# Performance work log

Measured on AMD Instinct MI355X. Metric: run time of the kernel, lower is better.

The kernel has to match this reference:

```python
import jax, jax.numpy as jnp
import numpy as np

N_EMBD = 448
HEAD_SIZE = 64

def setup_inputs() -> dict:
    key = jax.random.key(0)
    k1, k2, k3, k4 = jax.random.split(key, 4)
    B, T = 16, 2048
    x = jax.random.normal(k1, (B, T, N_EMBD), dtype=jnp.float32)
    # nn.Linear(n_embd, head_size, bias=False): weight shape (head_size, n_embd); y = x @ W.T
    s = 1.0 / np.sqrt(N_EMBD)
    Wk = jax.random.uniform(k2, (HEAD_SIZE, N_EMBD), jnp.float32, -s, s)
    Wq = jax.random.uniform(k3, (HEAD_SIZE, N_EMBD), jnp.float32, -s, s)
    Wv = jax.random.uniform(k4, (HEAD_SIZE, N_EMBD), jnp.float32, -s, s)
    return {"x": x, "Wk": Wk, "Wq": Wq, "Wv": Wv}

def reference(x, Wk, Wq, Wv):
    B, T, C = x.shape
    k = jnp.einsum('btc,hc->bth', x, Wk)  # (B,T,H)
    q = jnp.einsum('btc,hc->bth', x, Wq)
    v = jnp.einsum('btc,hc->bth', x, Wv)
    scale = 1.0 / jnp.sqrt(jnp.float32(C))  # NOTE: scales by sqrt(n_embd), as in source
    wei = jnp.einsum('bth,bsh->bts', q, k) * scale  # (B,T,T)
    causal = jnp.tril(jnp.ones((T, T), dtype=bool))
    wei = jnp.where(causal[None, :, :], wei, -jnp.inf)
    wei = jax.nn.softmax(wei, axis=-1)
    # dropout is identity in eval mode
    out = jnp.einsum('bts,bsh->bth', wei, v)  # (B,T,H)
    return out
```

## Files before the change

### kernel.cpp

```cpp
#include <hip/hip_runtime.h>
#include <math.h>

#define BT 32768
#define NC 448
#define NH 64
#define TT 2048

typedef __bf16 bf16x8 __attribute__((ext_vector_type(8)));
typedef float  f32x4  __attribute__((ext_vector_type(4)));

__device__ __forceinline__ unsigned short f2bf(float f) {
  unsigned u = __builtin_bit_cast(unsigned, f);
  return (unsigned short)((u + 0x7FFFu + ((u >> 16) & 1u)) >> 16);
}
__device__ __forceinline__ ushort4 f2bf4(float4 v) {
  ushort4 b; b.x = f2bf(v.x); b.y = f2bf(v.y); b.z = f2bf(v.z); b.w = f2bf(v.w);
  return b;
}
__device__ __forceinline__ float bf2f(unsigned short u) {
  return __builtin_bit_cast(float, (unsigned)u << 16);
}


__global__ __launch_bounds__(256) void proj_kernel(
    const float* __restrict__ x, const float* __restrict__ Wk,
    const float* __restrict__ Wq, const float* __restrict__ Wv,
    unsigned short* __restrict__ kws, unsigned short* __restrict__ qws,
    unsigned short* __restrict__ vws)
{
  __shared__ unsigned short xs[2][4096];
  __shared__ unsigned short wsm[2][4096];
  const int tid = threadIdx.x;
  const int w = tid >> 6, lane = tid & 63;
  const int q = lane >> 4, l15 = lane & 15;
  const int r0 = blockIdx.x * 64;
  const int p = blockIdx.y;
  const float* W = (p == 0) ? Wk : ((p == 1) ? Wq : Wv);

  f32x4 acc[4];
#pragma unroll
  for (int i = 0; i < 4; ++i) acc[i] = f32x4{0.f, 0.f, 0.f, 0.f};

  const int c0 = (tid & 15) * 4, r_ = tid >> 4;

  float4 xr[4], wr[4];
#pragma unroll
  for (int i = 0; i < 4; ++i) {
    xr[i] = *(const float4*)&x[(size_t)(r0 + r_ + 16 * i) * NC + c0];
    wr[i] = *(const float4*)&W[(size_t)(r_ + 16 * i) * NC + c0];
  }

  for (int ch = 0; ch < 7; ++ch) {
    const int cur = ch & 1;
#pragma unroll
    for (int i = 0; i < 4; ++i) {
      int r = r_ + 16 * i;
      int off = r * 64 + (((c0 >> 3) ^ (r & 7)) << 3) + (c0 & 7);
      *(ushort4*)&xs[cur][off]  = f2bf4(xr[i]);
      *(ushort4*)&wsm[cur][off] = f2bf4(wr[i]);
    }
    __syncthreads();
    if (ch < 6) {
      int kc = (ch + 1) * 64;
#pragma unroll
      for (int i = 0; i < 4; ++i) {
        xr[i] = *(const float4*)&x[(size_t)(r0 + r_ + 16 * i) * NC + kc + c0];
        wr[i] = *(const float4*)&W[(size_t)(r_ + 16 * i) * NC + kc + c0];
      }
    }
#pragma unroll
    for (int ks = 0; ks < 2; ++ks) {
      int xrow = w * 16 + l15;
      int g = q + 4 * ks;
      bf16x8 xf = *(const bf16x8*)&xs[cur][xrow * 64 + ((g ^ (xrow & 7)) << 3)];
#pragma unroll
      for (int t = 0; t < 4; ++t) {
        int wrow = t * 16 + l15;
        bf16x8 wf = *(const bf16x8*)&wsm[cur][wrow * 64 + ((g ^ (wrow & 7)) << 3)];
        if (p == 0)
          acc[t] = __builtin_amdgcn_mfma_f32_16x16x32_bf16(wf, xf, acc[t], 0, 0, 0);
        else
          acc[t] = __builtin_amdgcn_mfma_f32_16x16x32_bf16(xf, wf, acc[t], 0, 0, 0);
      }
    }
  }

  const size_t tile = (size_t)blockIdx.x * 4096;
  if (p == 0) {
#pragma unroll
    for (int t = 0; t < 4; ++t) {
      int j = w * 16 + l15;
      ushort4 bb; bb.x = f2bf(acc[t][0]); bb.y = f2bf(acc[t][1]);
      bb.z = f2bf(acc[t][2]); bb.w = f2bf(acc[t][3]);
      *(ushort4*)&kws[tile + j * 64 + (((2 * t + (q >> 1)) ^ (j & 7)) << 3) + ((q & 1) << 2)] = bb;
    }
  } else if (p == 1) {
    const float qs = 0.068161075f;
#pragma unroll
    for (int t = 0; t < 4; ++t) {
      int h = t * 16 + l15;
#pragma unroll
      for (int rr = 0; rr < 4; ++rr) {
        int R = r0 + w * 16 + q * 4 + rr;
        qws[(size_t)R * 64 + h] = f2bf(acc[t][rr] * qs);
      }
    }
  } else {
#pragma unroll
    for (int t = 0; t < 4; ++t) {
      int h = t * 16 + l15;
      ushort4 bb; bb.x = f2bf(acc[t][0]); bb.y = f2bf(acc[t][1]);
      bb.z = f2bf(acc[t][2]); bb.w = f2bf(acc[t][3]);
      *(ushort4*)&vws[tile + h * 64 + (((2 * w + (q >> 1)) ^ (h & 7)) << 3) + ((q & 1) << 2)] = bb;
    }
  }
}

__global__ __launch_bounds__(256) void attn_partial(
    const unsigned short* __restrict__ kws, const unsigned short* __restrict__ qws,
    const unsigned short* __restrict__ vws, float* __restrict__ out,
    unsigned short* __restrict__ opart, float* __restrict__ mlpart)
{
  __shared__ unsigned short ksm[2][4096];
  __shared__ unsigned short vtm[2][4096];
  __shared__ unsigned short psm[4096];
  const int bx = blockIdx.x, b = blockIdx.y;
  int qt, kt0, ktn, ci; bool direct;
  if (bx < 16)      { qt = 16 + bx; kt0 = 0;  ktn = 16;     ci = 0; direct = false; }
  else if (bx < 32) { qt = 47 - bx; kt0 = 16; ktn = qt + 1; ci = 1; direct = false; }
  else              { qt = 47 - bx; kt0 = 0;  ktn = qt + 1; ci = 0; direct = true;  }
  const int nt = ktn - kt0;

  const int tid = threadIdx.x;
  const int w = tid >> 6, lane = tid & 63;
  const int q = lane >> 4, l15 = lane & 15;
  const int t0 = b * TT + qt * 64;
  const int l7 = l15 & 7;

  bf16x8 qf[2];
#pragma unroll
  for (int ks = 0; ks < 2; ++ks)
    qf[ks] = *(const bf16x8*)&qws[(size_t)(t0 + w * 16 + l15) * 64 + 32 * ks + q * 8];

  f32x4 oacc[4];
#pragma unroll
  for (int ht = 0; ht < 4; ++ht) oacc[ht] = f32x4{0.f, 0.f, 0.f, 0.f};
  float m_i = -INFINITY, l_i = 0.f;

  uint4 kr0, kr1, vr0, vr1;
  {
    const unsigned short* kt_ = kws + (size_t)(b * 32 + kt0) * 4096;
    const unsigned short* vt_ = vws + (size_t)(b * 32 + kt0) * 4096;
    kr0 = *(const uint4*)&kt_[tid * 8];  kr1 = *(const uint4*)&kt_[2048 + tid * 8];
    vr0 = *(const uint4*)&vt_[tid * 8];  vr1 = *(const uint4*)&vt_[2048 + tid * 8];
  }

  for (int it = 0; it < nt; ++it) {
    const int kt = kt0 + it;
    const int cur = it & 1;
    *(uint4*)&ksm[cur][tid * 8] = kr0;  *(uint4*)&ksm[cur][2048 + tid * 8] = kr1;
    *(uint4*)&vtm[cur][tid * 8] = vr0;  *(uint4*)&vtm[cur][2048 + tid * 8] = vr1;
    __syncthreads();
    if (it + 1 < nt) {
      const unsigned short* kt_ = kws + (size_t)(b * 32 + kt + 1) * 4096;
      const unsigned short* vt_ = vws + (size_t)(b * 32 + kt + 1) * 4096;
      kr0 = *(const uint4*)&kt_[tid * 8];  kr1 = *(const uint4*)&kt_[2048 + tid * 8];
      vr0 = *(const uint4*)&vt_[tid * 8];  vr1 = *(const uint4*)&vt_[2048 + tid * 8];
    }

    f32x4 sacc[4];
#pragma unroll
    for (int jt = 0; jt < 4; ++jt) sacc[jt] = f32x4{0.f, 0.f, 0.f, 0.f};
#pragma unroll
    for (int jt = 0; jt < 4; ++jt) {
      int j = jt * 16 + l15;
#pragma unroll
      for (int ks = 0; ks < 2; ++ks) {
        bf16x8 kf = *(const bf16x8*)&ksm[cur][j * 64 + (((q + 4 * ks) ^ (j & 7)) << 3)];
        sacc[jt] = __builtin_amdgcn_mfma_f32_16x16x32_bf16(kf, qf[ks], sacc[jt], 0, 0, 0);
      }
    }

    if (kt == qt) {
      int iloc = w * 16 + l15;
#pragma unroll
      for (int jt = 0; jt < 4; ++jt)
#pragma unroll
        for (int rr = 0; rr < 4; ++rr)
          if (jt * 16 + q * 4 + rr > iloc) sacc[jt][rr] = -INFINITY;
    }

    float mx = -INFINITY;
#pragma unroll
    for (int jt = 0; jt < 4; ++jt)
#pragma unroll
      for (int rr = 0; rr < 4; ++rr) mx = fmaxf(mx, sacc[jt][rr]);
    mx = fmaxf(mx, __shfl_xor(mx, 16));
    mx = fmaxf(mx, __shfl_xor(mx, 32));
    float mn = fmaxf(m_i, mx);
    float alpha = exp2f(m_i - mn);
    m_i = mn;
    float p[4][4], rs = 0.f;
#pragma unroll
    for (int jt = 0; jt < 4; ++jt)
#pragma unroll
      for (int rr = 0; rr < 4; ++rr) {
        float pv = exp2f(sacc[jt][rr] - mn);
        p[jt][rr] = pv; rs += pv;
      }
    rs += __shfl_xor(rs, 16);
    rs += __shfl_xor(rs, 32);
    l_i = l_i * alpha + rs;

    float a_t[4];
#pragma unroll
    for (int rr = 0; rr < 4; ++rr) a_t[rr] = __shfl(alpha, q * 4 + rr);
#pragma unroll
    for (int ht = 0; ht < 4; ++ht)
#pragma unroll
      for (int rr = 0; rr < 4; ++rr) oacc[ht][rr] *= a_t[rr];

    {
      int row = w * 16 + l15;
#pragma unroll
      for (int jt = 0; jt < 4; ++jt) {
        ushort4 bb; bb.x = f2bf(p[jt][0]); bb.y = f2bf(p[jt][1]);
        bb.z = f2bf(p[jt][2]); bb.w = f2bf(p[jt][3]);
        *(ushort4*)&psm[row * 64 + (((2 * jt + (q >> 1)) ^ l7) << 3) + ((q & 1) << 2)] = bb;
      }
    }

#pragma unroll
    for (int ks2 = 0; ks2 < 2; ++ks2) {
      int prow = w * 16 + l15;
      bf16x8 pf = *(const bf16x8*)&psm[prow * 64 + (((q + 4 * ks2) ^ l7) << 3)];
#pragma unroll
      for (int ht = 0; ht < 4; ++ht) {
        int h = ht * 16 + l15;
        bf16x8 vf = *(const bf16x8*)&vtm[cur][h * 64 + (((q + 4 * ks2) ^ l7) << 3)];
        oacc[ht] = __builtin_amdgcn_mfma_f32_16x16x32_bf16(pf, vf, oacc[ht], 0, 0, 0);
      }
    }
  }

  if (direct) {
    float l_t[4];
#pragma unroll
    for (int rr = 0; rr < 4; ++rr) l_t[rr] = __shfl(l_i, q * 4 + rr);
#pragma unroll
    for (int rr = 0; rr < 4; ++rr) {
      float inv = 1.f / l_t[rr];
      int R = t0 + w * 16 + q * 4 + rr;
#pragma unroll
      for (int ht = 0; ht < 4; ++ht)
        out[(size_t)R * 64 + ht * 16 + l15] = oacc[ht][rr] * inv;
    }
  } else {
    const size_t slot = (size_t)(b * 16 + (qt - 16)) * 2 + ci;
    unsigned short* Op = opart + slot * 4096;
#pragma unroll
    for (int rr = 0; rr < 4; ++rr) {
      int rloc = w * 16 + q * 4 + rr;
#pragma unroll
      for (int ht = 0; ht < 4; ++ht)
        Op[rloc * 64 + ht * 16 + l15] = f2bf(oacc[ht][rr]);
    }
    if (q == 0) {
      mlpart[slot * 128 + w * 16 + l15]      = m_i;
      mlpart[slot * 128 + 64 + w * 16 + l15] = l_i;
    }
  }
}

__global__ __launch_bounds__(256) void combine_kernel(
    const unsigned short* __restrict__ opart, const float* __restrict__ mlpart,
    float* __restrict__ out)
{
  const int qtc = blockIdx.x, b = blockIdx.y;
  const int qt = 16 + qtc;
  const int t = threadIdx.x;
  const int r = t >> 2, c0 = (t & 3) * 16;
  const size_t s0 = (size_t)(b * 16 + qtc) * 2;

  float m0 = mlpart[s0 * 128 + r],       l0 = mlpart[s0 * 128 + 64 + r];
  float m1 = mlpart[(s0 + 1) * 128 + r], l1 = mlpart[(s0 + 1) * 128 + 64 + r];
  float m  = fmaxf(m0, m1);
  float w0 = exp2f(m0 - m), w1 = exp2f(m1 - m);
  float inv = 1.f / (w0 * l0 + w1 * l1);
  w0 *= inv; w1 *= inv;

  const unsigned short* O0 = opart + s0 * 4096 + r * 64 + c0;
  const unsigned short* O1 = opart + (s0 + 1) * 4096 + r * 64 + c0;
  union { uint4 v; unsigned short e[8]; } a0, a1;
  float* op = out + (size_t)(b * TT + qt * 64 + r) * 64;
#pragma unroll
  for (int half = 0; half < 2; ++half) {
    a0.v = *(const uint4*)&O0[half * 8];
    a1.v = *(const uint4*)&O1[half * 8];
    float res[8];
#pragma unroll
    for (int u = 0; u < 8; ++u)
      res[u] = w0 * bf2f(a0.e[u]) + w1 * bf2f(a1.e[u]);
    *(float4*)&op[c0 + half * 8]     = make_float4(res[0], res[1], res[2], res[3]);
    *(float4*)&op[c0 + half * 8 + 4] = make_float4(res[4], res[5], res[6], res[7]);
  }
}

extern "C" void kernel_launch(void* const* d_in, const int* in_sizes, int n_in,
                              void* d_out, int out_size, void* d_ws, size_t ws_size,
                              hipStream_t stream) {
  const float* x  = (const float*)d_in[0];
  const float* Wk = (const float*)d_in[1];
  const float* Wq = (const float*)d_in[2];
  const float* Wv = (const float*)d_in[3];
  unsigned short* kws = (unsigned short*)d_ws;
  unsigned short* qws = kws + (size_t)BT * NH;
  unsigned short* vws = qws + (size_t)BT * NH;
  unsigned short* opart = vws + (size_t)BT * NH;
  float* mlpart = (float*)(opart + (size_t)512 * 4096);
  float* out = (float*)d_out;

  proj_kernel<<<dim3(512, 3), 256, 0, stream>>>(x, Wk, Wq, Wv, kws, qws, vws);
  attn_partial<<<dim3(48, 16), 256, 0, stream>>>(kws, qws, vws, out, opart, mlpart);
  combine_kernel<<<dim3(16, 16), 256, 0, stream>>>(opart, mlpart, out);
}
```

Baseline: 147.7 us.

## Fuse K/Q/V projections into one pass over x with prepacked bf16 weights

The projection kernel previously ran three grid slices, each reading and converting the same x tile for one weight matrix. Now one block computes all three projections from a single x tile in shared memory. A new small kernel prepacks the weights into bf16 fragment order so each wave loads its weight fragments straight into registers, which removes the weight staging through shared memory. The cost is an extra kernel launch, roughly three times more accumulator registers, fewer blocks (512 instead of 1536), and reuse of the opart workspace as scratch for the packed weights.

```diff
diff --git a/kernel.cpp b/kernel.cpp
--- a/kernel.cpp
+++ b/kernel.cpp
@@ -22,33 +22,53 @@
 }
 
 
+__global__ __launch_bounds__(256) void wprep_kernel(
+    const float* __restrict__ Wk, const float* __restrict__ Wq,
+    const float* __restrict__ Wv, unsigned short* __restrict__ wp)
+{
+  int idx = blockIdx.x * 256 + threadIdx.x;
+  int r = idx & 63;
+  int t = idx >> 6;
+  int g = t & 7; t >>= 3;
+  int ch = t % 7, p = t / 7;
+  const float* W = (p == 0) ? Wk : ((p == 1) ? Wq : Wv);
+  const float* src = &W[(size_t)r * NC + ch * 64 + g * 8];
+  float4 a = *(const float4*)src;
+  float4 b = *(const float4*)(src + 4);
+  *(ushort4*)&wp[(size_t)idx * 8]     = f2bf4(a);
+  *(ushort4*)&wp[(size_t)idx * 8 + 4] = f2bf4(b);
+}
+
 __global__ __launch_bounds__(256) void proj_kernel(
-    const float* __restrict__ x, const float* __restrict__ Wk,
-    const float* __restrict__ Wq, const float* __restrict__ Wv,
+    const float* __restrict__ x, const unsigned short* __restrict__ wp,
     unsigned short* __restrict__ kws, unsigned short* __restrict__ qws,
     unsigned short* __restrict__ vws)
 {
   __shared__ unsigned short xs[2][4096];
-  __shared__ unsigned short wsm[2][4096];
   const int tid = threadIdx.x;
   const int w = tid >> 6, lane = tid & 63;
   const int q = lane >> 4, l15 = lane & 15;
   const int r0 = blockIdx.x * 64;
-  const int p = blockIdx.y;
-  const float* W = (p == 0) ? Wk : ((p == 1) ? Wq : Wv);
-
-  f32x4 acc[4];
-#pragma unroll
-  for (int i = 0; i < 4; ++i) acc[i] = f32x4{0.f, 0.f, 0.f, 0.f};
+
+  f32x4 acc[3][4];
+#pragma unroll
+  for (int p = 0; p < 3; ++p)
+#pragma unroll
+    for (int t = 0; t < 4; ++t) acc[p][t] = f32x4{0.f, 0.f, 0.f, 0.f};
 
   const int c0 = (tid & 15) * 4, r_ = tid >> 4;
-
-  float4 xr[4], wr[4];
-#pragma unroll
-  for (int i = 0; i < 4; ++i) {
+  const int wbase = (w * 16 + l15) * 8;
+
+  float4 xr[4];
+  bf16x8 wfr[3][2], wnx[3][2];
+#pragma unroll
+  for (int i = 0; i < 4; ++i)
     xr[i] = *(const float4*)&x[(size_t)(r0 + r_ + 16 * i) * NC + c0];
-    wr[i] = *(const float4*)&W[(size_t)(r_ + 16 * i) * NC + c0];
-  }
+#pragma unroll
+  for (int p = 0; p < 3; ++p)
+#pragma unroll
+    for (int ks = 0; ks < 2; ++ks)
+      wfr[p][ks] = *(const bf16x8*)&wp[(size_t)((p * 7 + 0) * 8 + (q + 4 * ks)) * 512 + wbase];
 
   for (int ch = 0; ch < 7; ++ch) {
     const int cur = ch & 1;
@@ -56,62 +76,66 @@
     for (int i = 0; i < 4; ++i) {
       int r = r_ + 16 * i;
       int off = r * 64 + (((c0 >> 3) ^ (r & 7)) << 3) + (c0 & 7);
-      *(ushort4*)&xs[cur][off]  = f2bf4(xr[i]);
-      *(ushort4*)&wsm[cur][off] = f2bf4(wr[i]);
+      *(ushort4*)&xs[cur][off] = f2bf4(xr[i]);
     }
     __syncthreads();
     if (ch < 6) {
       int kc = (ch + 1) * 64;
 #pragma unroll
-      for (int i = 0; i < 4; ++i) {
+      for (int i = 0; i < 4; ++i)
         xr[i] = *(const float4*)&x[(size_t)(r0 + r_ + 16 * i) * NC + kc + c0];
-        wr[i] = *(const float4*)&W[(size_t)(r_ + 16 * i) * NC + kc + c0];
-      }
+#pragma unroll
+      for (int p = 0; p < 3; ++p)
+#pragma unroll
+        for (int ks = 0; ks < 2; ++ks)
+          wnx[p][ks] = *(const bf16x8*)&wp[(size_t)((p * 7 + ch + 1) * 8 + (q + 4 * ks)) * 512 + wbase];
     }
 #pragma unroll
     for (int ks = 0; ks < 2; ++ks) {
-      int xrow = w * 16 + l15;
-      int g = q + 4 * ks;
-      bf16x8 xf = *(const bf16x8*)&xs[cur][xrow * 64 + ((g ^ (xrow & 7)) << 3)];
 #pragma unroll
       for (int t = 0; t < 4; ++t) {
-        int wrow = t * 16 + l15;
-        bf16x8 wf = *(const bf16x8*)&wsm[cur][wrow * 64 + ((g ^ (wrow & 7)) << 3)];
-        if (p == 0)
-          acc[t] = __builtin_amdgcn_mfma_f32_16x16x32_bf16(wf, xf, acc[t], 0, 0, 0);
-        else
-          acc[t] = __builtin_amdgcn_mfma_f32_16x16x32_bf16(xf, wf, acc[t], 0, 0, 0);
-      }
+        int xrow = t * 16 + l15;
+        bf16x8 xf = *(const bf16x8*)&xs[cur][xrow * 64 + (((q + 4 * ks) ^ (xrow & 7)) << 3)];
+        acc[0][t] = __builtin_amdgcn_mfma_f32_16x16x32_bf16(wfr[0][ks], xf, acc[0][t], 0, 0, 0);
+        acc[1][t] = __builtin_amdgcn_mfma_f32_16x16x32_bf16(xf, wfr[1][ks], acc[1][t], 0, 0, 0);
+        acc[2][t] = __builtin_amdgcn_mfma_f32_16x16x32_bf16(xf, wfr[2][ks], acc[2][t], 0, 0, 0);
+      }
+    }
+    if (ch < 6) {
+#pragma unroll
+      for (int p = 0; p < 3; ++p)
+#pragma unroll
+        for (int ks = 0; ks < 2; ++ks)
+          wfr[p][ks] = wnx[p][ks];
     }
   }
 
   const size_t tile = (size_t)blockIdx.x * 4096;
-  if (p == 0) {
+#pragma unroll
+  for (int t = 0; t < 4; ++t) {
+    int j = t * 16 + l15;
+    ushort4 bb; bb.x = f2bf(acc[0][t][0]); bb.y = f2bf(acc[0][t][1]);
+    bb.z = f2bf(acc[0][t][2]); bb.w = f2bf(acc[0][t][3]);
+    *(ushort4*)&kws[tile + j * 64 + (((2 * w + (q >> 1)) ^ (j & 7)) << 3) + ((q & 1) << 2)] = bb;
+  }
+  {
+    const float qs = 0.068161075f;
+    int h = w * 16 + l15;
+#pragma unroll
+    for (int t = 0; t < 4; ++t)
+#pragma unroll
+      for (int rr = 0; rr < 4; ++rr) {
+        int R = r0 + t * 16 + q * 4 + rr;
+        qws[(size_t)R * 64 + h] = f2bf(acc[1][t][rr] * qs);
+      }
+  }
+  {
+    int h = w * 16 + l15;
 #pragma unroll
     for (int t = 0; t < 4; ++t) {
-      int j = w * 16 + l15;
-      ushort4 bb; bb.x = f2bf(acc[t][0]); bb.y = f2bf(acc[t][1]);
-      bb.z = f2bf(acc[t][2]); bb.w = f2bf(acc[t][3]);
-      *(ushort4*)&kws[tile + j * 64 + (((2 * t + (q >> 1)) ^ (j & 7)) << 3) + ((q & 1) << 2)] = bb;
-    }
-  } else if (p == 1) {
-    const float qs = 0.068161075f;
-#pragma unroll
-    for (int t = 0; t < 4; ++t) {
-      int h = t * 16 + l15;
-#pragma unroll
-      for (int rr = 0; rr < 4; ++rr) {
-        int R = r0 + w * 16 + q * 4 + rr;
-        qws[(size_t)R * 64 + h] = f2bf(acc[t][rr] * qs);
-      }
-    }
-  } else {
-#pragma unroll
-    for (int t = 0; t < 4; ++t) {
-      int h = t * 16 + l15;
-      ushort4 bb; bb.x = f2bf(acc[t][0]); bb.y = f2bf(acc[t][1]);
-      bb.z = f2bf(acc[t][2]); bb.w = f2bf(acc[t][3]);
-      *(ushort4*)&vws[tile + h * 64 + (((2 * w + (q >> 1)) ^ (h & 7)) << 3) + ((q & 1) << 2)] = bb;
+      ushort4 bb; bb.x = f2bf(acc[2][t][0]); bb.y = f2bf(acc[2][t][1]);
+      bb.z = f2bf(acc[2][t][2]); bb.w = f2bf(acc[2][t][3]);
+      *(ushort4*)&vws[tile + h * 64 + (((2 * t + (q >> 1)) ^ (h & 7)) << 3) + ((q & 1) << 2)] = bb;
     }
   }
 }
@@ -319,8 +343,10 @@
   unsigned short* opart = vws + (size_t)BT * NH;
   float* mlpart = (float*)(opart + (size_t)512 * 4096);
   float* out = (float*)d_out;
-
-  proj_kernel<<<dim3(512, 3), 256, 0, stream>>>(x, Wk, Wq, Wv, kws, qws, vws);
+  unsigned short* wprep = opart;
+
+  wprep_kernel<<<dim3(42), 256, 0, stream>>>(Wk, Wq, Wv, wprep);
+  proj_kernel<<<dim3(512), 256, 0, stream>>>(x, wprep, kws, qws, vws);
   attn_partial<<<dim3(48, 16), 256, 0, stream>>>(kws, qws, vws, out, opart, mlpart);
   combine_kernel<<<dim3(16, 16), 256, 0, stream>>>(opart, mlpart, out);
 }
```

New measurement: 142.1 us. 3.8% less time.
